# Kernel optimization log

Hardware: AMD Instinct MI355X
Metric: run time of the kernel (lower is better)

## Reference

```python
import jax, jax.numpy as jnp
import numpy as np

WS = 8        # window_size
SS = 4        # shift_size
HEADS = 4
DH = 32       # dim_head
SCALE = DH ** -0.5


def setup_inputs() -> dict:
    key = jax.random.key(0)
    k1, k2, k3 = jax.random.split(key, 3)
    B, C, H, W = 8, 128, 256, 256
    inner = HEADS * DH
    x = jax.random.normal(k1, (B, C, H, W), dtype=jnp.float32)
    w_qkv = jax.random.normal(k2, (C, 3 * inner), dtype=jnp.float32) * (C ** -0.5)
    w_proj = jax.random.normal(k3, (inner, C), dtype=jnp.float32) * (inner ** -0.5)
    b_proj = jnp.zeros((C,), dtype=jnp.float32)
    return {"x": x, "w_qkv": w_qkv, "w_proj": w_proj, "b_proj": b_proj}


def reference(x, w_qkv, w_proj, b_proj):
    B, C, H, W = x.shape
    # to channels-last and cyclic shift
    xh = jnp.transpose(x, (0, 2, 3, 1))                      # [B,H,W,C]
    xh = jnp.roll(xh, shift=(-SS, -SS), axis=(1, 2))
    # window partition -> [nW, ws*ws, C]
    nH, nW = H // WS, W // WS
    xw = xh.reshape(B, nH, WS, nW, WS, C)
    xw = jnp.transpose(xw, (0, 1, 3, 2, 4, 1 + 4)).reshape(B * nH * nW, WS * WS, C)
    # qkv
    qkv = xw @ w_qkv                                         # [nWin, L, 3*inner]
    q, k, v = jnp.split(qkv, 3, axis=-1)
    def heads(t):
        n, L, _ = t.shape
        return jnp.transpose(t.reshape(n, L, HEADS, DH), (0, 2, 1, 3))  # [n,h,L,dh]
    q, k, v = heads(q), heads(k), heads(v)
    attn = jax.nn.softmax(jnp.einsum('nhld,nhmd->nhlm', q, k) * SCALE, axis=-1)
    out = jnp.einsum('nhlm,nhmd->nhld', attn, v)             # [n,h,L,dh]
    n, _, L, _ = out.shape
    out = jnp.transpose(out, (0, 2, 1, 3)).reshape(n, L, HEADS * DH)
    out = out @ w_proj + b_proj                              # [n,L,C]
    # window reverse -> [B,H,W,C]
    out = out.reshape(B, nH, nW, WS, WS, C)
    out = jnp.transpose(out, (0, 1, 3, 2, 4, 5)).reshape(B, H, W, C)
    # reverse cyclic shift, back to channels-first
    out = jnp.roll(out, shift=(SS, SS), axis=(1, 2))
    return jnp.transpose(out, (0, 3, 1, 2))                  # [B,C,H,W]
```

## Files before the change

### kernel.cpp

```cpp
#include <hip/hip_runtime.h>


typedef __attribute__((ext_vector_type(8))) short bf16x8;
typedef __attribute__((ext_vector_type(4))) float f32x4;

__device__ __forceinline__ unsigned pk2(float lo, float hi) {
  union { float f; unsigned u; } a, b; a.f = lo; b.f = hi;
  return __builtin_amdgcn_perm(b.u + 0x8000u, a.u + 0x8000u, 0x07060302u);
}

__device__ __forceinline__ unsigned short f2bf_rne(float f) {
  union { float f; unsigned u; } v; v.f = f;
  return (unsigned short)((v.u + 0x7FFFu + ((v.u >> 16) & 1u)) >> 16);
}

__global__ void prep_kernel(const float* __restrict__ wqkv,
                            const float* __restrict__ wproj,
                            unsigned short* __restrict__ wT) {
  const int idx = blockIdx.x * 256 + (int)threadIdx.x;
  if (idx < 384 * 128) {
    const int n = idx >> 7, k = idx & 127;
    wT[idx] = f2bf_rne(wqkv[k * 384 + n]);
  } else {
    const int j = idx - 384 * 128;
    const int n = j >> 7, k = j & 127;
    wT[idx] = f2bf_rne(wproj[k * 128 + n]);
  }
}

__global__ void __launch_bounds__(256, 3)
swin_kernel(const float* __restrict__ x, const unsigned short* __restrict__ wT,
            const float* __restrict__ bproj, float* __restrict__ out) {
  __shared__ unsigned short SM[24576];

  const int bid = blockIdx.x;
  const int win = (bid & 7) * 1024 + (bid >> 3);
  const int b  = win >> 10;
  const int wy = (win >> 5) & 31;
  const int wx = win & 31;
  const int tid  = (int)threadIdx.x;
  const int lane = tid & 63;
  const int wv   = tid >> 6;
  const int q    = lane >> 4;
  const int l16  = lane & 15;
  const int qh   = q >> 1, ql = q & 1;

  unsigned short* XF  = SM;
  unsigned short* KFh = SM + 8192  + wv * 2048;
  unsigned short* VFh = SM + 16384 + wv * 2048;
  unsigned short* QFh = XF + wv * 2048;

  {
    const int t4 = tid & 15;
    const int a  = tid >> 4;
    const int ty = t4 >> 1, txb = (t4 & 1) << 2;
    const int hh = (wy * 8 + ty + 4) & 255;
    const int ww = (wx * 8 + txb + 4) & 255;
    const float* src = x + ((b * 128) * 256 + hh) * 256 + ww;
    const int t0 = t4 << 2;
#pragma unroll
    for (int i = 0; i < 2; ++i) {
      const int c0 = a * 4 + i * 64;
      const float4 v0 = *(const float4*)(src + (c0    ) * 65536);
      const float4 v1 = *(const float4*)(src + (c0 + 1) * 65536);
      const float4 v2 = *(const float4*)(src + (c0 + 2) * 65536);
      const float4 v3 = *(const float4*)(src + (c0 + 3) * 65536);
      unsigned short* p = &XF[(c0 >> 3) * 512 + t0 * 8 + (c0 & 7)];
      uint2 w;
      w.x = pk2(v0.x, v1.x); w.y = pk2(v2.x, v3.x);
      *(uint2*)(p + 0)  = w;
      w.x = pk2(v0.y, v1.y); w.y = pk2(v2.y, v3.y);
      *(uint2*)(p + 8)  = w;
      w.x = pk2(v0.z, v1.z); w.y = pk2(v2.z, v3.z);
      *(uint2*)(p + 16) = w;
      w.x = pk2(v0.w, v1.w); w.y = pk2(v2.w, v3.w);
      *(uint2*)(p + 24) = w;
    }
  }
  __syncthreads();

  f32x4 aQT[2][4] = {}; f32x4 aKT[2][4] = {};
#pragma unroll
  for (int ks = 0; ks < 4; ++ks) {
    const int ko = ks * 32 + q * 8;
    bf16x8 xb[4];
#pragma unroll
    for (int nt = 0; nt < 4; ++nt)
      xb[nt] = *(const bf16x8*)&XF[(ks * 4 + q) * 512 + (nt * 16 + l16) * 8];
#pragma unroll
    for (int mA = 0; mA < 2; ++mA) {
      const int row = wv * 32 + mA * 16 + l16;
      const bf16x8 wq = *(const bf16x8*)&wT[row * 128 + ko];
      const bf16x8 wk = *(const bf16x8*)&wT[(128 + row) * 128 + ko];
      __builtin_amdgcn_s_setprio(1);
#pragma unroll
      for (int nt = 0; nt < 4; ++nt) {
        aQT[mA][nt] = __builtin_amdgcn_mfma_f32_16x16x32_bf16(wq, xb[nt], aQT[mA][nt], 0, 0, 0);
        aKT[mA][nt] = __builtin_amdgcn_mfma_f32_16x16x32_bf16(wk, xb[nt], aKT[mA][nt], 0, 0, 0);
      }
      __builtin_amdgcn_s_setprio(0);
    }
  }
#pragma unroll
  for (int mA = 0; mA < 2; ++mA)
#pragma unroll
    for (int nt = 0; nt < 4; ++nt) {
      uint2 w;
      w.x = pk2(aKT[mA][nt][0], aKT[mA][nt][1]);
      w.y = pk2(aKT[mA][nt][2], aKT[mA][nt][3]);
      *(uint2*)&KFh[(mA * 2 + qh) * 512 + (nt * 16 + l16) * 8 + ql * 4] = w;
    }

  f32x4 aV[4][2] = {};
#pragma unroll
  for (int ks = 0; ks < 4; ++ks) {
    const int ko = ks * 32 + q * 8;
    bf16x8 af[4];
#pragma unroll
    for (int mt = 0; mt < 4; ++mt)
      af[mt] = *(const bf16x8*)&XF[(ks * 4 + q) * 512 + (mt * 16 + l16) * 8];
#pragma unroll
    for (int nt = 0; nt < 2; ++nt) {
      const bf16x8 bv = *(const bf16x8*)&wT[(256 + wv * 32 + nt * 16 + l16) * 128 + ko];
      __builtin_amdgcn_s_setprio(1);
#pragma unroll
      for (int mt = 0; mt < 4; ++mt)
        aV[mt][nt] = __builtin_amdgcn_mfma_f32_16x16x32_bf16(af[mt], bv, aV[mt][nt], 0, 0, 0);
      __builtin_amdgcn_s_setprio(0);
    }
  }
#pragma unroll
  for (int mt = 0; mt < 4; ++mt)
#pragma unroll
    for (int nt = 0; nt < 2; ++nt) {
      uint2 w;
      w.x = pk2(aV[mt][nt][0], aV[mt][nt][1]);
      w.y = pk2(aV[mt][nt][2], aV[mt][nt][3]);
      *(uint2*)&VFh[(mt * 2 + qh) * 256 + (nt * 16 + l16) * 8 + ql * 4] = w;
    }
  __syncthreads();

  constexpr float SC = 0.17677669529663687f * 1.4426950408889634f;
#pragma unroll
  for (int mA = 0; mA < 2; ++mA)
#pragma unroll
    for (int nt = 0; nt < 4; ++nt) {
      uint2 w;
      w.x = pk2(aQT[mA][nt][0] * SC, aQT[mA][nt][1] * SC);
      w.y = pk2(aQT[mA][nt][2] * SC, aQT[mA][nt][3] * SC);
      *(uint2*)&QFh[(mA * 2 + qh) * 512 + (nt * 16 + l16) * 8 + ql * 4] = w;
    }

  bf16x8 kf[4], qf[4];
#pragma unroll
  for (int t = 0; t < 4; ++t) {
    kf[t] = *(const bf16x8*)&KFh[q * 512 + (t * 16 + l16) * 8];
    qf[t] = *(const bf16x8*)&QFh[q * 512 + (t * 16 + l16) * 8];
  }
  f32x4 aS[4][4] = {};
  __builtin_amdgcn_s_setprio(1);
#pragma unroll
  for (int mt = 0; mt < 4; ++mt)
#pragma unroll
    for (int nt = 0; nt < 4; ++nt)
      aS[mt][nt] = __builtin_amdgcn_mfma_f32_16x16x32_bf16(kf[mt], qf[nt], aS[mt][nt], 0, 0, 0);
  __builtin_amdgcn_s_setprio(0);

#pragma unroll
  for (int mt = 0; mt < 4; ++mt)
#pragma unroll
    for (int nt = 0; nt < 4; ++nt)
#pragma unroll
      for (int r = 0; r < 4; ++r)
        aS[mt][nt][r] = __builtin_amdgcn_exp2f(aS[mt][nt][r]);
  float inv[4];
#pragma unroll
  for (int nt = 0; nt < 4; ++nt) {
    float s = 0.f;
#pragma unroll
    for (int mt = 0; mt < 4; ++mt)
#pragma unroll
      for (int r = 0; r < 4; ++r) s += aS[mt][nt][r];
    s += __shfl_xor(s, 16);
    s += __shfl_xor(s, 32);
    inv[nt] = 1.0f / s;
  }

  f32x4 aOT[2][4] = {};
#pragma unroll
  for (int h = 0; h < 2; ++h) {
#pragma unroll
    for (int mh = 0; mh < 2; ++mh) {
      const int mt = h * 2 + mh;
#pragma unroll
      for (int nt = 0; nt < 4; ++nt) {
        uint2 w;
        w.x = pk2(aS[mt][nt][0], aS[mt][nt][1]);
        w.y = pk2(aS[mt][nt][2], aS[mt][nt][3]);
        *(uint2*)&QFh[(mh * 2 + qh) * 512 + (nt * 16 + l16) * 8 + ql * 4] = w;
      }
    }
    bf16x8 pf[4], vf[2];
#pragma unroll
    for (int t = 0; t < 4; ++t)
      pf[t] = *(const bf16x8*)&QFh[q * 512 + (t * 16 + l16) * 8];
#pragma unroll
    for (int nb = 0; nb < 2; ++nb)
      vf[nb] = *(const bf16x8*)&VFh[(h * 4 + q) * 256 + (nb * 16 + l16) * 8];
    __builtin_amdgcn_s_setprio(1);
#pragma unroll
    for (int mo = 0; mo < 2; ++mo)
#pragma unroll
      for (int np = 0; np < 4; ++np)
        aOT[mo][np] = __builtin_amdgcn_mfma_f32_16x16x32_bf16(vf[mo], pf[np], aOT[mo][np], 0, 0, 0);
    __builtin_amdgcn_s_setprio(0);
  }

#pragma unroll
  for (int mo = 0; mo < 2; ++mo)
#pragma unroll
    for (int np = 0; np < 4; ++np) {
      const float s = inv[np];
      uint2 w;
      w.x = pk2(aOT[mo][np][0] * s, aOT[mo][np][1] * s);
      w.y = pk2(aOT[mo][np][2] * s, aOT[mo][np][3] * s);
      *(uint2*)&XF[(wv * 4 + mo * 2 + qh) * 512 + (np * 16 + l16) * 8 + ql * 4] = w;
    }
  __syncthreads();

  f32x4 aP[4][2] = {};
#pragma unroll
  for (int ks = 0; ks < 4; ++ks) {
    const int ko = ks * 32 + q * 8;
    bf16x8 af[4];
#pragma unroll
    for (int mt = 0; mt < 4; ++mt)
      af[mt] = *(const bf16x8*)&XF[(ks * 4 + q) * 512 + (mt * 16 + l16) * 8];
#pragma unroll
    for (int nt = 0; nt < 2; ++nt) {
      const bf16x8 bw = *(const bf16x8*)&wT[(384 + wv * 32 + nt * 16 + l16) * 128 + ko];
      __builtin_amdgcn_s_setprio(1);
#pragma unroll
      for (int mt = 0; mt < 4; ++mt)
        aP[mt][nt] = __builtin_amdgcn_mfma_f32_16x16x32_bf16(af[mt], bw, aP[mt][nt], 0, 0, 0);
      __builtin_amdgcn_s_setprio(0);
    }
  }
#pragma unroll
  for (int nt = 0; nt < 2; ++nt) {
    const int c = wv * 32 + nt * 16 + l16;
    const float bias = bproj[c];
#pragma unroll
    for (int mt = 0; mt < 4; ++mt) {
      const int tb  = mt * 16 + q * 4;
      const int ty  = tb >> 3;
      const int txb = tb & 7;
      const int hh  = (wy * 8 + ty + 4) & 255;
      const int ww  = (wx * 8 + txb + 4) & 255;
      float4 v;
      v.x = aP[mt][nt][0] + bias;
      v.y = aP[mt][nt][1] + bias;
      v.z = aP[mt][nt][2] + bias;
      v.w = aP[mt][nt][3] + bias;
      *(float4*)(out + ((b * 128 + c) * 256 + hh) * 256 + ww) = v;
    }
  }
}

extern "C" void kernel_launch(void* const* d_in, const int* in_sizes, int n_in,
                              void* d_out, int out_size, void* d_ws, size_t ws_size,
                              hipStream_t stream) {
  const float* x     = (const float*)d_in[0];
  const float* wqkv  = (const float*)d_in[1];
  const float* wproj = (const float*)d_in[2];
  const float* bp    = (const float*)d_in[3];
  unsigned short* wT = (unsigned short*)d_ws;

  prep_kernel<<<256, 256, 0, stream>>>(wqkv, wproj, wT);
  swin_kernel<<<8192, 256, 0, stream>>>(x, wT, bp, (float*)d_out);
}
```

Baseline: 608.5 us.

## Share K/V shared-memory scratch and chunk scores to raise occupancy

```diff
diff --git a/kernel.cpp b/kernel.cpp
--- a/kernel.cpp
+++ b/kernel.cpp
@@ -28,10 +28,10 @@
   }
 }
 
-__global__ void __launch_bounds__(256, 3)
+__global__ void __launch_bounds__(256, 4)
 swin_kernel(const float* __restrict__ x, const unsigned short* __restrict__ wT,
             const float* __restrict__ bproj, float* __restrict__ out) {
-  __shared__ unsigned short SM[24576];
+  __shared__ unsigned short SM[16384];
 
   const int bid = blockIdx.x;
   const int win = (bid & 7) * 1024 + (bid >> 3);
@@ -46,8 +46,7 @@
   const int qh   = q >> 1, ql = q & 1;
 
   unsigned short* XF  = SM;
-  unsigned short* KFh = SM + 8192  + wv * 2048;
-  unsigned short* VFh = SM + 16384 + wv * 2048;
+  unsigned short* SCh = SM + 8192 + wv * 2048;
   unsigned short* QFh = XF + wv * 2048;
 
   {
@@ -108,8 +107,13 @@
       uint2 w;
       w.x = pk2(aKT[mA][nt][0], aKT[mA][nt][1]);
       w.y = pk2(aKT[mA][nt][2], aKT[mA][nt][3]);
-      *(uint2*)&KFh[(mA * 2 + qh) * 512 + (nt * 16 + l16) * 8 + ql * 4] = w;
-    }
+      *(uint2*)&SCh[(mA * 2 + qh) * 512 + (nt * 16 + l16) * 8 + ql * 4] = w;
+    }
+  bf16x8 kf[4];
+#pragma unroll
+  for (int t = 0; t < 4; ++t)
+    kf[t] = *(const bf16x8*)&SCh[q * 512 + (t * 16 + l16) * 8];
+  asm volatile("" ::: "memory");
 
   f32x4 aV[4][2] = {};
 #pragma unroll
@@ -136,7 +140,7 @@
       uint2 w;
       w.x = pk2(aV[mt][nt][0], aV[mt][nt][1]);
       w.y = pk2(aV[mt][nt][2], aV[mt][nt][3]);
-      *(uint2*)&VFh[(mt * 2 + qh) * 256 + (nt * 16 + l16) * 8 + ql * 4] = w;
+      *(uint2*)&SCh[(mt * 2 + qh) * 256 + (nt * 16 + l16) * 8 + ql * 4] = w;
     }
   __syncthreads();
 
@@ -150,70 +154,58 @@
       w.y = pk2(aQT[mA][nt][2] * SC, aQT[mA][nt][3] * SC);
       *(uint2*)&QFh[(mA * 2 + qh) * 512 + (nt * 16 + l16) * 8 + ql * 4] = w;
     }
-
-  bf16x8 kf[4], qf[4];
-#pragma unroll
-  for (int t = 0; t < 4; ++t) {
-    kf[t] = *(const bf16x8*)&KFh[q * 512 + (t * 16 + l16) * 8];
+  bf16x8 qf[4];
+#pragma unroll
+  for (int t = 0; t < 4; ++t)
     qf[t] = *(const bf16x8*)&QFh[q * 512 + (t * 16 + l16) * 8];
-  }
-  f32x4 aS[4][4] = {};
-  __builtin_amdgcn_s_setprio(1);
-#pragma unroll
-  for (int mt = 0; mt < 4; ++mt)
-#pragma unroll
-    for (int nt = 0; nt < 4; ++nt)
-      aS[mt][nt] = __builtin_amdgcn_mfma_f32_16x16x32_bf16(kf[mt], qf[nt], aS[mt][nt], 0, 0, 0);
-  __builtin_amdgcn_s_setprio(0);
-
-#pragma unroll
-  for (int mt = 0; mt < 4; ++mt)
-#pragma unroll
-    for (int nt = 0; nt < 4; ++nt)
-#pragma unroll
-      for (int r = 0; r < 4; ++r)
-        aS[mt][nt][r] = __builtin_amdgcn_exp2f(aS[mt][nt][r]);
+
+  f32x4 aOT[2][4] = {};
+  float sacc[4] = {0.f, 0.f, 0.f, 0.f};
+#pragma unroll
+  for (int h = 0; h < 2; ++h) {
+    f32x4 aSh[2][4] = {};
+    __builtin_amdgcn_s_setprio(1);
+#pragma unroll
+    for (int mh = 0; mh < 2; ++mh)
+#pragma unroll
+      for (int nt = 0; nt < 4; ++nt)
+        aSh[mh][nt] = __builtin_amdgcn_mfma_f32_16x16x32_bf16(kf[h * 2 + mh], qf[nt], aSh[mh][nt], 0, 0, 0);
+    __builtin_amdgcn_s_setprio(0);
+#pragma unroll
+    for (int mh = 0; mh < 2; ++mh)
+#pragma unroll
+      for (int nt = 0; nt < 4; ++nt) {
+#pragma unroll
+        for (int r = 0; r < 4; ++r)
+          aSh[mh][nt][r] = __builtin_amdgcn_exp2f(aSh[mh][nt][r]);
+        sacc[nt] += aSh[mh][nt][0] + aSh[mh][nt][1] + aSh[mh][nt][2] + aSh[mh][nt][3];
+        uint2 w;
+        w.x = pk2(aSh[mh][nt][0], aSh[mh][nt][1]);
+        w.y = pk2(aSh[mh][nt][2], aSh[mh][nt][3]);
+        *(uint2*)&QFh[(mh * 2 + qh) * 512 + (nt * 16 + l16) * 8 + ql * 4] = w;
+      }
+    bf16x8 pf[4], vf[2];
+#pragma unroll
+    for (int t = 0; t < 4; ++t)
+      pf[t] = *(const bf16x8*)&QFh[q * 512 + (t * 16 + l16) * 8];
+#pragma unroll
+    for (int nb = 0; nb < 2; ++nb)
+      vf[nb] = *(const bf16x8*)&SCh[(h * 4 + q) * 256 + (nb * 16 + l16) * 8];
+    __builtin_amdgcn_s_setprio(1);
+#pragma unroll
+    for (int mo = 0; mo < 2; ++mo)
+#pragma unroll
+      for (int np = 0; np < 4; ++np)
+        aOT[mo][np] = __builtin_amdgcn_mfma_f32_16x16x32_bf16(vf[mo], pf[np], aOT[mo][np], 0, 0, 0);
+    __builtin_amdgcn_s_setprio(0);
+  }
   float inv[4];
 #pragma unroll
   for (int nt = 0; nt < 4; ++nt) {
-    float s = 0.f;
-#pragma unroll
-    for (int mt = 0; mt < 4; ++mt)
-#pragma unroll
-      for (int r = 0; r < 4; ++r) s += aS[mt][nt][r];
+    float s = sacc[nt];
     s += __shfl_xor(s, 16);
     s += __shfl_xor(s, 32);
     inv[nt] = 1.0f / s;
-  }
-
-  f32x4 aOT[2][4] = {};
-#pragma unroll
-  for (int h = 0; h < 2; ++h) {
-#pragma unroll
-    for (int mh = 0; mh < 2; ++mh) {
-      const int mt = h * 2 + mh;
-#pragma unroll
-      for (int nt = 0; nt < 4; ++nt) {
-        uint2 w;
-        w.x = pk2(aS[mt][nt][0], aS[mt][nt][1]);
-        w.y = pk2(aS[mt][nt][2], aS[mt][nt][3]);
-        *(uint2*)&QFh[(mh * 2 + qh) * 512 + (nt * 16 + l16) * 8 + ql * 4] = w;
-      }
-    }
-    bf16x8 pf[4], vf[2];
-#pragma unroll
-    for (int t = 0; t < 4; ++t)
-      pf[t] = *(const bf16x8*)&QFh[q * 512 + (t * 16 + l16) * 8];
-#pragma unroll
-    for (int nb = 0; nb < 2; ++nb)
-      vf[nb] = *(const bf16x8*)&VFh[(h * 4 + q) * 256 + (nb * 16 + l16) * 8];
-    __builtin_amdgcn_s_setprio(1);
-#pragma unroll
-    for (int mo = 0; mo < 2; ++mo)
-#pragma unroll
-      for (int np = 0; np < 4; ++np)
-        aOT[mo][np] = __builtin_amdgcn_mfma_f32_16x16x32_bf16(vf[mo], pf[np], aOT[mo][np], 0, 0, 0);
-    __builtin_amdgcn_s_setprio(0);
   }
 
 #pragma unroll
```

Result: no change. 607.8 us (-0.1%).
